# Kernel tuning notes

Hardware: AMD Instinct MI355X
Metric: run time of the kernel (lower is better)

The kernel has to match this reference:

```python
import jax, jax.numpy as jnp
import numpy as np
from jax import lax
from jax.scipy.special import logsumexp

B, T, L, K = 4, 512, 96, 64  # batch, sample_size, num_label, segment_max_len
W = K - 1                    # number of non-zero-start segment lengths considered
NEG = -1e30


def setup_inputs() -> dict:
    key = jax.random.key(0)
    k1, k2 = jax.random.split(key)
    segment_score = jax.random.normal(k1, (B, T, T, L), dtype=jnp.float32)
    transitions = jax.random.uniform(k2, (L + 1, L), dtype=jnp.float32)  # row L = BOS
    return {"segment_score": segment_score, "transitions": transitions}


def _log_z(segment_score, transitions):
    dtype = segment_score.dtype
    trans = transitions[:L]   # [Lp, Lc]
    bos = transitions[L]      # [Lc]
    # NOTE: original code stores exp(...) (not log) for frame 0 -- preserved faithfully.
    alpha0 = jnp.zeros((B, T, L), dtype)
    alpha0 = alpha0.at[:, 0, :].set(jnp.exp(segment_score[:, 0, 0, :] + bos[None, :]))

    w = jnp.arange(1, W + 1, dtype=dtype)  # weight (j+1) per window slot
    jidx = jnp.arange(W)

    def step(alpha, t):
        # scores of all segments ending at frame t: [B, T(start), L]
        seg_t = lax.dynamic_slice(segment_score, (0, 0, t, 0), (B, T, 1, L))[:, :, 0, :]
        base = jnp.maximum(t - W, 0)
        m = jnp.minimum(t, W)  # number of valid non-zero-start entries
        # window slot j: start frame = base+1+j, prev alpha frame = base+j, weight = j+1
        seg_win = lax.dynamic_slice(seg_t, (0, base + 1, 0), (B, W, L))      # [B,W,Lc]
        alpha_win = lax.dynamic_slice(alpha, (0, base, 0), (B, W, L))        # [B,W,Lp]
        total = (alpha_win[:, :, :, None]
                 + (seg_win * w[None, :, None])[:, :, None, :]
                 + (trans[None, :, :] * w[:, None, None])[None, :, :, :])    # [B,W,Lp,Lc]
        total = jnp.where(jidx[None, :, None, None] < m, total, NEG)
        # zero-start segment (only when t+1 <= K i.e. t <= W)
        tlen = (t + 1).astype(dtype)
        z = seg_t[:, 0, :] * tlen + bos[None, :] * tlen                       # [B,Lc]
        z = jnp.where(t <= W, z, NEG)
        cat = jnp.concatenate([total.reshape(B, W * L, L), z[:, None, :]], axis=1)
        new = logsumexp(cat, axis=1)                                          # [B,Lc]
        alpha = lax.dynamic_update_slice(alpha, new[:, None, :], (0, t, 0))
        return alpha, None

    alpha, _ = lax.scan(step, alpha0, jnp.arange(1, T))
    return logsumexp(alpha[:, T - 1, :], axis=1)  # [B]


def reference(segment_score, transitions):
    return _log_z(segment_score, transitions)
```

## Files before the change

kernel.cpp:

```cpp
#include <hip/hip_runtime.h>


#define Tn 512
#define Ln 96
#define HL 48
#define LSQ (Ln * Ln)
#define Wn 63
#define KCH 8
#define NROLE 46
#define NEGINF (-1e30f)
#define SENT 0x7FC00000u

#define AGENT __HIP_MEMORY_SCOPE_AGENT
#define WG __HIP_MEMORY_SCOPE_WORKGROUP
#define RLX __ATOMIC_RELAXED
#define LDSF() asm volatile("s_waitcnt lgkmcnt(0)" ::: "memory")
#define CBAR() asm volatile("" ::: "memory")
#define BARRIER()                 \
  do {                            \
    LDSF();                       \
    CBAR();                       \
    __builtin_amdgcn_s_barrier(); \
    CBAR();                       \
  } while (0)
#define SIDX(b, i, t) ((((size_t)(b) * Tn + (i)) * Tn + (t)) * Ln)

typedef unsigned long long u64;
typedef unsigned int u32;
typedef unsigned short u16;

__device__ __forceinline__ float wsumred(float v) {
#pragma unroll
  for (int m = 32; m >= 1; m >>= 1) v += __shfl_xor(v, m, 64);
  return v;
}
__device__ __forceinline__ u64 pack2(float lo, float hi) {
  return (u64)__float_as_uint(lo) | ((u64)__float_as_uint(hi) << 32);
}
__device__ __forceinline__ u16 tobf16(float x) {
  return (u16)((__float_as_uint(x) + 0x8000u) >> 16);
}
__device__ __forceinline__ float wavemax48(float v) {
  int x;
  x = __builtin_amdgcn_update_dpp(__float_as_int(v), __float_as_int(v), 0xB1,
                                  0xF, 0xF, false);
  v = fmaxf(v, __int_as_float(x));
  x = __builtin_amdgcn_update_dpp(__float_as_int(v), __float_as_int(v), 0x4E,
                                  0xF, 0xF, false);
  v = fmaxf(v, __int_as_float(x));
  x = __builtin_amdgcn_update_dpp(__float_as_int(v), __float_as_int(v), 0x141,
                                  0xF, 0xF, false);
  v = fmaxf(v, __int_as_float(x));
  x = __builtin_amdgcn_update_dpp(__float_as_int(v), __float_as_int(v), 0x140,
                                  0xF, 0xF, false);
  v = fmaxf(v, __int_as_float(x));
  float r0 = __int_as_float(__builtin_amdgcn_readlane(__float_as_int(v), 0));
  float r1 = __int_as_float(__builtin_amdgcn_readlane(__float_as_int(v), 16));
  float r2 = __int_as_float(__builtin_amdgcn_readlane(__float_as_int(v), 32));
  float r3 = __int_as_float(__builtin_amdgcn_readlane(__float_as_int(v), 48));
  return fmaxf(fmaxf(r0, r1), fmaxf(r2, r3));
}
__device__ __forceinline__ float comb(float Slo, float Shi, float C0, float C1,
                                      float wseg) {
  const float Cm = fmaxf(C0, C1);
  return Cm + wseg + __logf(__expf(C0 - Cm) * Slo + __expf(C1 - Cm) * Shi);
}

#define MV1(SRC, RR, SLO, SHI)                                       \
  float SLO, SHI;                                                    \
  {                                                                  \
    const float4* A4 = (const float4*)(SRC);                         \
    float a0 = 0, a1 = 0, a2 = 0, a3 = 0;                            \
    _Pragma("unroll") for (int q = 0; q < 12; ++q) {                 \
      float4 a = A4[q];                                              \
      a0 = fmaf(a.x, RR[4 * q + 0], a0);                             \
      a1 = fmaf(a.y, RR[4 * q + 1], a1);                             \
      a2 = fmaf(a.z, RR[4 * q + 2], a2);                             \
      a3 = fmaf(a.w, RR[4 * q + 3], a3);                             \
    }                                                                \
    SLO = (a0 + a1) + (a2 + a3);                                     \
    float b0 = 0, b1 = 0, b2 = 0, b3 = 0;                            \
    _Pragma("unroll") for (int q = 12; q < 24; ++q) {                \
      float4 a = A4[q];                                              \
      b0 = fmaf(a.x, RR[4 * q + 0], b0);                             \
      b1 = fmaf(a.y, RR[4 * q + 1], b1);                             \
      b2 = fmaf(a.z, RR[4 * q + 2], b2);                             \
      b3 = fmaf(a.w, RR[4 * q + 3], b3);                             \
    }                                                                \
    SHI = (b0 + b1) + (b2 + b3);                                     \
  }

#define MVB(SRC, RR, SLO, SHI)                                               \
  float SLO, SHI;                                                            \
  {                                                                          \
    const uint4* A4 = (const uint4*)(SRC);                                   \
    float a0 = 0, a1 = 0, a2 = 0, a3 = 0;                                    \
    _Pragma("unroll") for (int q = 0; q < 6; ++q) {                          \
      uint4 a = A4[q];                                                       \
      a0 = fmaf(__uint_as_float(a.x << 16), RR[8 * q + 0], a0);              \
      a1 = fmaf(__uint_as_float(a.x & 0xFFFF0000u), RR[8 * q + 1], a1);      \
      a2 = fmaf(__uint_as_float(a.y << 16), RR[8 * q + 2], a2);              \
      a3 = fmaf(__uint_as_float(a.y & 0xFFFF0000u), RR[8 * q + 3], a3);      \
      a0 = fmaf(__uint_as_float(a.z << 16), RR[8 * q + 4], a0);              \
      a1 = fmaf(__uint_as_float(a.z & 0xFFFF0000u), RR[8 * q + 5], a1);      \
      a2 = fmaf(__uint_as_float(a.w << 16), RR[8 * q + 6], a2);              \
      a3 = fmaf(__uint_as_float(a.w & 0xFFFF0000u), RR[8 * q + 7], a3);      \
    }                                                                        \
    SLO = (a0 + a1) + (a2 + a3);                                             \
    float b0 = 0, b1 = 0, b2 = 0, b3 = 0;                                    \
    _Pragma("unroll") for (int q = 6; q < 12; ++q) {                         \
      uint4 a = A4[q];                                                       \
      b0 = fmaf(__uint_as_float(a.x << 16), RR[8 * q + 0], b0);              \
      b1 = fmaf(__uint_as_float(a.x & 0xFFFF0000u), RR[8 * q + 1], b1);      \
      b2 = fmaf(__uint_as_float(a.y << 16), RR[8 * q + 2], b2);              \
      b3 = fmaf(__uint_as_float(a.y & 0xFFFF0000u), RR[8 * q + 3], b3);      \
      b0 = fmaf(__uint_as_float(a.z << 16), RR[8 * q + 4], b0);              \
      b1 = fmaf(__uint_as_float(a.z & 0xFFFF0000u), RR[8 * q + 5], b1);      \
      b2 = fmaf(__uint_as_float(a.w << 16), RR[8 * q + 6], b2);              \
      b3 = fmaf(__uint_as_float(a.w & 0xFFFF0000u), RR[8 * q + 7], b3);      \
    }                                                                        \
    SHI = (b0 + b1) + (b2 + b3);                                             \
  }

__global__ void init_ws(u64* ws) {
  const size_t n1 = (size_t)4 * Tn * Ln;
  const size_t n = n1 * 9;
  for (size_t i = (size_t)blockIdx.x * blockDim.x + threadIdx.x; i < n;
       i += (size_t)gridDim.x * blockDim.x)
    ws[i] = (i < n1) ? (((u64)SENT) << 32) : 0ull;
}

__global__ __launch_bounds__(512, 1) void semicrf(
    const float* __restrict__ seg, const float* __restrict__ tr,
    float* __restrict__ out, u64* axp, u64* acc) {
  const int b = blockIdx.x / NROLE;
  const int role = blockIdx.x % NROLE;
  const int tid = threadIdx.x;

  __shared__ __align__(16) float E[LSQ];
  __shared__ __align__(16) u16 AlbRh[8][Ln];
  __shared__ float CRng[8][2];
  __shared__ __align__(16) float slotC2[4][Ln];
  __shared__ __align__(16) float slotC3[4][Ln];
  __shared__ float RESTm[4][Ln];
  __shared__ float RESTv[4][Ln];
  __shared__ __align__(16) float Alb_s[4][2][Ln];
  __shared__ float CstS[4][2][2];
  __shared__ float redbuf[2];
  __shared__ int stg[4][2];

  if (tid < 8) stg[tid >> 1][tid & 1] = -1;
  for (int i = tid; i < LSQ; i += 512) E[i] = __expf(tr[i]);
  __syncthreads();

  if (role != 0) {
    const int pair = tid >> 7;
    const int tp = tid & 127;
    const int wv = tp >> 6;
    const int rl = tp & 63;
    const bool act = rl < HL;
    const int lab = wv * HL + (act ? rl : HL - 1);
    const int pu = (role - 1) * 4 + pair;
    const int d = 4 + pu / 3;
    const int m3 = pu % 3;
    const int j = d & 7;
    u64* chain = acc + (size_t)(j * 4 + b) * Tn * Ln;
    const u64* axB = axp + (size_t)b * Tn * Ln;
    float R[Ln];
#pragma unroll
    for (int lp = 0; lp < Ln; ++lp) R[lp] = E[lp * Ln + lab];
    int wc = 1;
    const bool aHead = (d + KCH > Wn);
    const int t0 = d + ((m3 - (d % 3)) + 3) % 3;
    int bufi = 0;

    for (int t = t0; t < Tn; t += 3) {
      const int s = t - d;
      const int w = (t <= Wn) ? (s + 1) : (64 - d);
      while (w > wc) {
        ++wc;
#pragma unroll
        for (int lp = 0; lp < Ln; ++lp) R[lp] *= E[lp * Ln + lab];
      }
      const float segv = seg[SIDX(b, s + 1, t) + lab];
      const size_t tIdx = (size_t)t * Ln + lab;
      const bool head = aHead || (s < KCH);
      u64 ua = 0;
      if (!head) ua = __hip_atomic_load(&chain[tIdx], RLX, AGENT);

      u64 up = __hip_atomic_load(&axB[(size_t)s * Ln + lab], RLX, AGENT);
      while ((u32)(up >> 32) == SENT)
        up = __hip_atomic_load(&axB[(size_t)s * Ln + lab], RLX, AGENT);

      if (act) Alb_s[pair][bufi][lab] = __uint_as_float((u32)up);
      if (rl == 0) CstS[pair][bufi][wv] = __uint_as_float((u32)(up >> 32));
      LDSF();
      __hip_atomic_store(&stg[pair][wv], t, RLX, WG);
      while (__hip_atomic_load(&stg[pair][wv ^ 1], RLX, WG) < t) {}
      CBAR();
      const float C0 = CstS[pair][bufi][0], C1 = CstS[pair][bufi][1];
      MV1(Alb_s[pair][bufi], R, Slo, Shi)
      const float c = comb(Slo, Shi, C0, C1, (float)w * segv);
      bufi ^= 1;

      float m, v;
      if (head) {
        m = c;
        v = 1.f;
      } else {
        while (((ua >> 32) & 0xFFu) != (u32)(d + KCH))
          ua = __hip_atomic_load(&chain[tIdx], RLX, AGENT);
        const float pm = __uint_as_float((u32)ua);
        const float pv = __uint_as_float(((u32)(ua >> 32)) & ~0xFFu);
        const float nm = fmaxf(pm, c);
        v = pv * __expf(pm - nm) + __expf(c - nm);
        m = nm;
      }
      if (act) {
        const u32 vb = (__float_as_uint(v) & ~0xFFu) | (u32)d;
        __hip_atomic_store(&chain[tIdx],
                           (u64)__float_as_uint(m) | ((u64)vb << 32), RLX,
                           AGENT);
      }
    }
    return;
  }

  const int w6 = tid >> 6;
  const int l = tid & 63;
  const bool act = l < HL;
  const int h = w6 & 1;
  const int lab = h * HL + (act ? l : HL - 1);
  u64* axpB = axp + (size_t)b * Tn * Ln;
  const float bos = tr[LSQ + lab];

  if (w6 < 2) {
    float R1[Ln];
#pragma unroll
    for (int lp = 0; lp < Ln; ++lp) R1[lp] = E[lp * Ln + lab];
    int w1c = 1;
    float q0 = seg[SIDX(b, 1, 1) + lab];
    float q1 = seg[SIDX(b, 2, 2) + lab];
    {
      const float a0 = __expf(seg[SIDX(b, 0, 0) + lab] + bos);
      const float Cw = wavemax48(act ? a0 : NEGINF);
      const float ax0 = __expf(a0 - Cw);
      if (act) __hip_atomic_store(&axpB[lab], pack2(ax0, Cw), RLX, AGENT);
      if (act) AlbRh[0][lab] = tobf16(ax0);
      if (l == 0) CRng[0][h] = Cw;
    }
    BARRIER();

    float lastAx = 0.f, lastCw = 0.f;
    for (int t = 1; t < Tn; ++t) {
      const float s1 = q0;
      q0 = q1;
      if (t + 2 < Tn) q1 = seg[SIDX(b, t + 2, t + 2) + lab];
      const int w1 = (t <= Wn) ? t : Wn;
      if (w1 > w1c) {
        w1c = w1;
#pragma unroll
        for (int lp = 0; lp < Ln; ++lp) R1[lp] *= E[lp * Ln + lab];
      }
      const float C0 = CRng[(t - 1) & 7][0], C1 = CRng[(t - 1) & 7][1];
      MVB(AlbRh[(t - 1) & 7], R1, Slo, Shi)
      const float c1 = comb(Slo, Shi, C0, C1, (float)w1 * s1);
      const float c2 = (t >= 2) ? slotC2[t & 3][lab] : NEGINF;
      const float c3 = (t >= 3) ? slotC3[t & 3][lab] : NEGINF;
      const float mr = RESTm[t & 3][lab], vr = RESTv[t & 3][lab];
      const float M = fmaxf(fmaxf(c1, c2), fmaxf(c3, mr));
      const float vs = __expf(c1 - M) + __expf(c2 - M) + __expf(c3 - M) +
                       vr * __expf(mr - M);
      const float alpha = M + __logf(vs);
      const float Cw = wavemax48(act ? alpha : NEGINF);
      const float axn = __expf(alpha - Cw);
      if (act)
        __hip_atomic_store(&axpB[(size_t)t * Ln + lab], pack2(axn, Cw), RLX,
                           AGENT);
      if (act) AlbRh[t & 7][lab] = tobf16(axn);
      if (l == 0) CRng[t & 7][h] = Cw;
      lastAx = axn;
      lastCw = Cw;
      BARRIER();
    }
    const float sm = wsumred(act ? lastAx : 0.f);
    if (l == 0) redbuf[h] = lastCw + __logf(sm);
    BARRIER();
    if (w6 == 0 && l == 0) {
      const float G0 = redbuf[0], G1 = redbuf[1];
      const float Mx = fmaxf(G0, G1);
      out[b] = Mx + __logf(__expf(G0 - Mx) + __expf(G1 - Mx));
    }
    return;
  }

  if (w6 < 4) {
    float R2[Ln];
#pragma unroll
    for (int lp = 0; lp < Ln; ++lp) R2[lp] = E[lp * Ln + lab];
    int wc = 1;
    float q0 = seg[SIDX(b, 1, 2) + lab];
    float q1 = seg[SIDX(b, 2, 3) + lab];
    BARRIER();
    for (int t = 1; t < Tn; ++t) {
      const int tp1 = t + 1;
      if (tp1 < Tn) {
        const float sv = q0;
        q0 = q1;
        if (tp1 + 2 < Tn) q1 = seg[SIDX(b, tp1 + 1, tp1 + 2) + lab];
        const int w = (tp1 <= Wn) ? (tp1 - 1) : 62;
        if (w > wc) {
          wc = w;
#pragma unroll
          for (int lp = 0; lp < Ln; ++lp) R2[lp] *= E[lp * Ln + lab];
        }
        const float C0 = CRng[(t - 1) & 7][0], C1 = CRng[(t - 1) & 7][1];
        MVB(AlbRh[(t - 1) & 7], R2, Slo, Shi)
        const float c = comb(Slo, Shi, C0, C1, (float)w * sv);
        if (act) slotC2[tp1 & 3][lab] = c;
      }
      BARRIER();
    }
    BARRIER();
    return;
  }

  if (w6 < 6) {
    float R3[Ln];
#pragma unroll
    for (int lp = 0; lp < Ln; ++lp) R3[lp] = E[lp * Ln + lab];
    int wc = 1;
    float q0 = 0.f;
    float q1 = seg[SIDX(b, 1, 3) + lab];
    BARRIER();
    for (int t = 1; t < Tn; ++t) {
      const int tp1 = t + 1;
      if (tp1 < Tn) {
        const float sv = q0;
        q0 = q1;
        if (tp1 + 2 < Tn) q1 = seg[SIDX(b, tp1, tp1 + 2) + lab];
        if (tp1 >= 3) {
          const int w = (tp1 <= Wn) ? (tp1 - 2) : 61;
          if (w > wc) {
            wc = w;
#pragma unroll
            for (int lp = 0; lp < Ln; ++lp) R3[lp] *= E[lp * Ln + lab];
          }
          const float C0 = CRng[(t - 2) & 7][0], C1 = CRng[(t - 2) & 7][1];
          MVB(AlbRh[(t - 2) & 7], R3, Slo, Shi)
          const float c = comb(Slo, Shi, C0, C1, (float)w * sv);
          if (act) slotC3[tp1 & 3][lab] = c;
        }
      }
      BARRIER();
    }
    BARRIER();
    return;
  }

  {
    const int endd[8] = {8, 9, 10, 11, 4, 5, 6, 7};
    u64 UA[8], UB[8];
#pragma unroll
    for (int jj = 0; jj < 8; ++jj) {
      UA[jj] = 0;
      UB[jj] = 0;
    }
    float zq0 = seg[SIDX(b, 0, 2) + lab];
    float zq1 = seg[SIDX(b, 0, 3) + lab];
    {
      const float zv = 2.f * (seg[SIDX(b, 0, 1) + lab] + bos);
      if (act) {
        RESTm[1][lab] = zv;
        RESTv[1][lab] = 1.f;
      }
    }
    BARRIER();

#define RESTSTEP(U)                                                          \
  {                                                                          \
    float M = zv;                                                            \
    float em[8], ev[8];                                                      \
    _Pragma("unroll") for (int jj = 0; jj < 8; ++jj) {                       \
      if (tp1 >= endd[jj]) {                                                 \
        const size_t aIdx = (((size_t)jj * 4 + b) * Tn + tp1) * Ln + lab;    \
        while (((U[jj] >> 32) & 0xFFu) != (u32)endd[jj])                     \
          U[jj] = __hip_atomic_load(&acc[aIdx], RLX, AGENT);                 \
        em[jj] = __uint_as_float((u32)U[jj]);                                \
        ev[jj] = __uint_as_float(((u32)(U[jj] >> 32)) & ~0xFFu);             \
        M = fmaxf(M, em[jj]);                                                \
      } else {                                                               \
        em[jj] = NEGINF;                                                     \
        ev[jj] = 0.f;                                                        \
      }                                                                      \
    }                                                                        \
    float vs = __expf(zv - M);                                               \
    _Pragma("unroll") for (int jj = 0; jj < 8; ++jj) vs +=                   \
        ev[jj] * __expf(em[jj] - M);                                         \
    if (act) {                                                               \
      RESTm[tp1 & 3][lab] = M;                                               \
      RESTv[tp1 & 3][lab] = vs;                                              \
    }                                                                        \
    if (tp1 + 2 < Tn) {                                                      \
      _Pragma("unroll") for (int jj = 0; jj < 8; ++jj) {                     \
        if (tp1 + 2 >= endd[jj])                                             \
          U[jj] = __hip_atomic_load(                                         \
              &acc[(((size_t)jj * 4 + b) * Tn + (tp1 + 2)) * Ln + lab], RLX, \
              AGENT);                                                        \
      }                                                                      \
    }                                                                        \
  }

    for (int t = 1; t < Tn; ++t) {
      const int tp1 = t + 1;
      if (tp1 < Tn) {
        const float zv =
            (tp1 <= Wn) ? (float)(tp1 + 1) * (zq0 + bos) : NEGINF;
        zq0 = zq1;
        if (tp1 + 2 <= Wn) zq1 = seg[SIDX(b, 0, tp1 + 2) + lab];
        if (tp1 & 1) {
          RESTSTEP(UA)
        } else {
          RESTSTEP(UB)
        }
      }
      BARRIER();
    }
    BARRIER();
    return;
  }
}

extern "C" void kernel_launch(void* const* d_in, const int* in_sizes, int n_in,
                              void* d_out, int out_size, void* d_ws,
                              size_t ws_size, hipStream_t stream) {
  const float* seg = (const float*)d_in[0];
  const float* tr = (const float*)d_in[1];
  float* out = (float*)d_out;

  u64* axp = (u64*)d_ws;
  u64* acc = axp + (size_t)4 * Tn * Ln;

  hipLaunchKernelGGL(init_ws, dim3(2048), dim3(256), 0, stream, (u64*)d_ws);
  hipLaunchKernelGGL(semicrf, dim3(4 * NROLE), dim3(512), 0, stream, seg, tr,
                     out, axp, acc);
}
```

Measured before the change: 757.2 us.

## Add a fourth in-block lag stage for distance-4 segments, rebalancing helper roles

```diff
diff --git a/kernel.cpp b/kernel.cpp
--- a/kernel.cpp
+++ b/kernel.cpp
@@ -7,7 +7,7 @@
 #define LSQ (Ln * Ln)
 #define Wn 63
 #define KCH 8
-#define NROLE 46
+#define NROLE 37
 #define NEGINF (-1e30f)
 #define SENT 0x7FC00000u
 
@@ -130,7 +130,7 @@
     ws[i] = (i < n1) ? (((u64)SENT) << 32) : 0ull;
 }
 
-__global__ __launch_bounds__(512, 1) void semicrf(
+__global__ __launch_bounds__(640, 1) void semicrf(
     const float* __restrict__ seg, const float* __restrict__ tr,
     float* __restrict__ out, u64* axp, u64* acc) {
   const int b = blockIdx.x / NROLE;
@@ -142,15 +142,16 @@
   __shared__ float CRng[8][2];
   __shared__ __align__(16) float slotC2[4][Ln];
   __shared__ __align__(16) float slotC3[4][Ln];
+  __shared__ __align__(16) float slotC4[4][Ln];
   __shared__ float RESTm[4][Ln];
   __shared__ float RESTv[4][Ln];
-  __shared__ __align__(16) float Alb_s[4][2][Ln];
-  __shared__ float CstS[4][2][2];
+  __shared__ __align__(16) float Alb_s[5][2][Ln];
+  __shared__ float CstS[5][2][2];
   __shared__ float redbuf[2];
-  __shared__ int stg[4][2];
-
-  if (tid < 8) stg[tid >> 1][tid & 1] = -1;
-  for (int i = tid; i < LSQ; i += 512) E[i] = __expf(tr[i]);
+  __shared__ int stg[5][2];
+
+  if (tid < 10) stg[tid >> 1][tid & 1] = -1;
+  for (int i = tid; i < LSQ; i += 640) E[i] = __expf(tr[i]);
   __syncthreads();
 
   if (role != 0) {
@@ -160,8 +161,9 @@
     const int rl = tp & 63;
     const bool act = rl < HL;
     const int lab = wv * HL + (act ? rl : HL - 1);
-    const int pu = (role - 1) * 4 + pair;
-    const int d = 4 + pu / 3;
+    const int pu = (role - 1) * 5 + pair;
+    if (pu >= 177) return;
+    const int d = 5 + pu / 3;
     const int m3 = pu % 3;
     const int j = d & 7;
     u64* chain = acc + (size_t)(j * 4 + b) * Tn * Ln;
@@ -226,15 +228,15 @@
     return;
   }
 
-  const int w6 = tid >> 6;
+  const int w10 = tid >> 6;
   const int l = tid & 63;
   const bool act = l < HL;
-  const int h = w6 & 1;
+  const int h = w10 & 1;
   const int lab = h * HL + (act ? l : HL - 1);
   u64* axpB = axp + (size_t)b * Tn * Ln;
   const float bos = tr[LSQ + lab];
 
-  if (w6 < 2) {
+  if (w10 < 2) {
     float R1[Ln];
 #pragma unroll
     for (int lp = 0; lp < Ln; ++lp) R1[lp] = E[lp * Ln + lab];
@@ -267,10 +269,12 @@
       const float c1 = comb(Slo, Shi, C0, C1, (float)w1 * s1);
       const float c2 = (t >= 2) ? slotC2[t & 3][lab] : NEGINF;
       const float c3 = (t >= 3) ? slotC3[t & 3][lab] : NEGINF;
+      const float c4 = (t >= 4) ? slotC4[t & 3][lab] : NEGINF;
       const float mr = RESTm[t & 3][lab], vr = RESTv[t & 3][lab];
-      const float M = fmaxf(fmaxf(c1, c2), fmaxf(c3, mr));
+      const float M =
+          fmaxf(fmaxf(fmaxf(c1, c2), fmaxf(c3, c4)), mr);
       const float vs = __expf(c1 - M) + __expf(c2 - M) + __expf(c3 - M) +
-                       vr * __expf(mr - M);
+                       __expf(c4 - M) + vr * __expf(mr - M);
       const float alpha = M + __logf(vs);
       const float Cw = wavemax48(act ? alpha : NEGINF);
       const float axn = __expf(alpha - Cw);
@@ -286,7 +290,7 @@
     const float sm = wsumred(act ? lastAx : 0.f);
     if (l == 0) redbuf[h] = lastCw + __logf(sm);
     BARRIER();
-    if (w6 == 0 && l == 0) {
+    if (w10 == 0 && l == 0) {
       const float G0 = redbuf[0], G1 = redbuf[1];
       const float Mx = fmaxf(G0, G1);
       out[b] = Mx + __logf(__expf(G0 - Mx) + __expf(G1 - Mx));
@@ -294,7 +298,7 @@
     return;
   }
 
-  if (w6 < 4) {
+  if (w10 < 4) {
     float R2[Ln];
 #pragma unroll
     for (int lp = 0; lp < Ln; ++lp) R2[lp] = E[lp * Ln + lab];
@@ -325,7 +329,7 @@
     return;
   }
 
-  if (w6 < 6) {
+  if (w10 < 6) {
     float R3[Ln];
 #pragma unroll
     for (int lp = 0; lp < Ln; ++lp) R3[lp] = E[lp * Ln + lab];
@@ -358,8 +362,42 @@
     return;
   }
 
+  if (w10 < 8) {
+    float R4[Ln];
+#pragma unroll
+    for (int lp = 0; lp < Ln; ++lp) R4[lp] = E[lp * Ln + lab];
+    int wc = 1;
+    float q0 = 0.f;
+    float q1 = seg[SIDX(b, 1, 4) + lab];
+    BARRIER();
+    BARRIER();
+    for (int t = 2; t < Tn; ++t) {
+      const int tp1 = t + 1;
+      if (tp1 < Tn) {
+        const float sv = q0;
+        q0 = q1;
+        if (tp1 + 2 < Tn) q1 = seg[SIDX(b, tp1 - 2, tp1 + 2) + lab];
+        if (tp1 >= 4) {
+          const int w = (tp1 <= Wn) ? (tp1 - 3) : 60;
+          if (w > wc) {
+            wc = w;
+#pragma unroll
+            for (int lp = 0; lp < Ln; ++lp) R4[lp] *= E[lp * Ln + lab];
+          }
+          const float C0 = CRng[(t - 3) & 7][0], C1 = CRng[(t - 3) & 7][1];
+          MVB(AlbRh[(t - 3) & 7], R4, Slo, Shi)
+          const float c = comb(Slo, Shi, C0, C1, (float)w * sv);
+          if (act) slotC4[tp1 & 3][lab] = c;
+        }
+      }
+      BARRIER();
+    }
+    BARRIER();
+    return;
+  }
+
   {
-    const int endd[8] = {8, 9, 10, 11, 4, 5, 6, 7};
+    const int endd[8] = {8, 9, 10, 11, 12, 5, 6, 7};
     u64 UA[8], UB[8];
 #pragma unroll
     for (int jj = 0; jj < 8; ++jj) {
@@ -414,8 +452,7 @@
     for (int t = 1; t < Tn; ++t) {
       const int tp1 = t + 1;
       if (tp1 < Tn) {
-        const float zv =
-            (tp1 <= Wn) ? (float)(tp1 + 1) * (zq0 + bos) : NEGINF;
+        const float zv = (tp1 <= Wn) ? (float)(tp1 + 1) * (zq0 + bos) : NEGINF;
         zq0 = zq1;
         if (tp1 + 2 <= Wn) zq1 = seg[SIDX(b, 0, tp1 + 2) + lab];
         if (tp1 & 1) {
@@ -442,6 +479,6 @@
   u64* acc = axp + (size_t)4 * Tn * Ln;
 
   hipLaunchKernelGGL(init_ws, dim3(2048), dim3(256), 0, stream, (u64*)d_ws);
-  hipLaunchKernelGGL(semicrf, dim3(4 * NROLE), dim3(512), 0, stream, seg, tr,
+  hipLaunchKernelGGL(semicrf, dim3(4 * NROLE), dim3(640), 0, stream, seg, tr,
                      out, axp, acc);
 }
```

Result: slower. 1.323 ms (+74.7%).
